# Kernel tuning notes

Hardware: AMD Instinct MI355X
Metric: run time of the kernel (lower is better)

Reference implementation:

```python
import jax, jax.numpy as jnp
import numpy as np

B, N, DH = 256, 32, 128      # batch, n_agents, per-agent hidden
E = 496                       # n_edges (fully connected over 32 agents)
DIM_IN = 2 * DH               # 256, MLP input (concat of two agent states)
DIM_HID = 256
A = 12                        # dim_act
R = 4                         # payoff_rank
DIM_OUT = 2 * R * A           # 96


def setup_inputs() -> dict:
    key = jax.random.key(0)
    ks = jax.random.split(key, 7)
    hidden_states_n = jax.random.normal(ks[0], (B, N, DH), dtype=jnp.float32)
    edges_from = jax.random.randint(ks[1], (E,), 0, N, dtype=jnp.int32).astype(jnp.int64)
    edges_to = jax.random.randint(ks[2], (E,), 0, N, dtype=jnp.int32).astype(jnp.int64)
    # torch.nn.Linear params: W [out, in], b [out]
    W1 = jax.random.normal(ks[3], (DIM_HID, DIM_IN), dtype=jnp.float32) * (1.0 / np.sqrt(DIM_IN))
    b1 = jnp.zeros((DIM_HID,), dtype=jnp.float32)
    W2 = jax.random.normal(ks[4], (DIM_OUT, DIM_HID), dtype=jnp.float32) * (1.0 / np.sqrt(DIM_HID))
    b2 = jnp.zeros((DIM_OUT,), dtype=jnp.float32)
    return {"hidden_states_n": hidden_states_n, "W1": W1, "b1": b1, "W2": W2,
            "b2": b2, "edges_from": edges_from, "edges_to": edges_to}


def reference(hidden_states_n, W1, b1, W2, b2, edges_from, edges_to):
    hf = hidden_states_n[:, edges_from]                     # [B, E, DH]
    ht = hidden_states_n[:, edges_to]                       # [B, E, DH]
    # stack of (from||to, to||from): [2, B, E, 2*DH]
    inp = jnp.stack([jnp.concatenate([hf, ht], axis=-1),
                     jnp.concatenate([ht, hf], axis=-1)], axis=0)
    h = jax.nn.relu(inp @ W1.T + b1)                        # [2, B, E, DIM_HID]
    p = h @ W2.T + b2                                       # [2, B, E, 2*R*A]
    p = p.reshape(2, B, E, R, 2, A)
    # low-rank outer product per rank, summed over ranks: [2, B, E, A, A]
    payoffs = jnp.einsum('sberi,sberj->sbeij', p[..., 0, :], p[..., 1, :])
    # second copy is transposed, then mean over the two directions
    return 0.5 * (payoffs[0] + jnp.swapaxes(payoffs[1], -1, -2))  # [B, E, A, A]
```

## Files before the change

kernel.cpp:

```cpp
#include <hip/hip_runtime.h>

typedef unsigned int uint;
typedef _Float16 f16;

typedef __attribute__((ext_vector_type(8))) _Float16 f16x8;
typedef __attribute__((ext_vector_type(2))) _Float16 f16x2;
typedef __attribute__((ext_vector_type(4))) float f32x4;

#define E_CNT 496

__device__ __forceinline__ uint pack2_f16(float lo, float hi) {
    union { f16x2 h; uint u; } r;
    r.h[0] = (_Float16)lo;
    r.h[1] = (_Float16)hi;
    return r.u;
}

__global__ __launch_bounds__(256) void x_kernel(
    const float* __restrict__ hidden, const float* __restrict__ W1,
    const float* __restrict__ b1, f16* __restrict__ Xout) {
    __shared__ __align__(16) float hs[64 * 132];

    const int tid = threadIdx.x;
    const int rowblock = blockIdx.x >> 2;
    const int g = blockIdx.x & 3;
    const int ln = tid & 63;
    const int waveId = tid >> 6;
    const int quad = ln >> 4;
    const int l16 = ln & 15;
    const int row0 = rowblock * 64;

    union FU { uint u[4]; f16x8 v; };
    FU wf[2][4];
    float bh[2][4];
    #pragma unroll
    for (int nt = 0; nt < 2; ++nt) {
        const int t = (g * 4 + waveId) * 2 + nt;
        const int half = t >> 4;
        const int htile = t & 15;
        const float* wrow = W1 + (htile * 16 + l16) * 256 + half * 128 + quad * 8;
        #pragma unroll
        for (int kk = 0; kk < 4; ++kk) {
            float4 v0 = *(const float4*)(wrow + kk * 32);
            float4 v1 = *(const float4*)(wrow + kk * 32 + 4);
            wf[nt][kk].u[0] = pack2_f16(v0.x, v0.y);
            wf[nt][kk].u[1] = pack2_f16(v0.z, v0.w);
            wf[nt][kk].u[2] = pack2_f16(v1.x, v1.y);
            wf[nt][kk].u[3] = pack2_f16(v1.z, v1.w);
        }
        #pragma unroll
        for (int r = 0; r < 4; ++r)
            bh[nt][r] = 0.5f * b1[htile * 16 + quad * 4 + r];
    }

    {
        const float* src = hidden + row0 * 128;
        #pragma unroll
        for (int it = 0; it < 8; ++it) {
            int idx = it * 256 + tid;
            int r = idx >> 5;
            int c4 = idx & 31;
            float4 v = *(const float4*)(src + idx * 4);
            *(float4*)&hs[r * 132 + c4 * 4] = v;
        }
    }
    __syncthreads();

    #pragma unroll
    for (int ch = 0; ch < 4; ++ch) {
        FU hf[4];
        const float* hrow = &hs[(ch * 16 + l16) * 132 + quad * 8];
        #pragma unroll
        for (int kk = 0; kk < 4; ++kk) {
            float4 v0 = *(const float4*)(hrow + kk * 32);
            float4 v1 = *(const float4*)(hrow + kk * 32 + 4);
            hf[kk].u[0] = pack2_f16(v0.x, v0.y);
            hf[kk].u[1] = pack2_f16(v0.z, v0.w);
            hf[kk].u[2] = pack2_f16(v1.x, v1.y);
            hf[kk].u[3] = pack2_f16(v1.z, v1.w);
        }
        #pragma unroll
        for (int nt = 0; nt < 2; ++nt) {
            const int t = (g * 4 + waveId) * 2 + nt;
            const int half = t >> 4;
            const int htile = t & 15;
            f32x4 acc = (f32x4){0.f, 0.f, 0.f, 0.f};
            #pragma unroll
            for (int kk = 0; kk < 4; ++kk)
                acc = __builtin_amdgcn_mfma_f32_16x16x32_f16(wf[nt][kk].v, hf[kk].v, acc, 0, 0, 0);
            uint2 o;
            o.x = pack2_f16(acc[0] + bh[nt][0], acc[1] + bh[nt][1]);
            o.y = pack2_f16(acc[2] + bh[nt][2], acc[3] + bh[nt][3]);
            f16* dst = Xout + half * (8192 * 256)
                     + (row0 + ch * 16 + l16) * 256 + htile * 16 + quad * 4;
            *(uint2*)dst = o;
        }
    }
}

#define PAIR_STRIDE 100
#define R_OFF 800
#define WAVE_PF 1600

__global__ __launch_bounds__(256, 4) void gemm_payoff_kernel(
    const f16* __restrict__ X1, const f16* __restrict__ X2,
    const int* __restrict__ e_f, const int* __restrict__ e_t,
    const float* __restrict__ W2, const float* __restrict__ b2,
    float* __restrict__ out) {

    __shared__ __align__(16) unsigned char smem[26624];
    f16* w2s = (f16*)smem;
    float* pf = (float*)smem;

    const int tid = threadIdx.x;
    const int ln = tid & 63;
    const int waveId = tid >> 6;
    const int quad = ln >> 4;
    const int l16 = ln & 15;
    const int pl = l16 & 7;
    const int s = l16 >> 3;

    const int bx = blockIdx.x;
    const int lb = (bx & 7) * 248 + (bx >> 3);

    bool f64 = true, t64 = true;
    #pragma unroll
    for (int i = 0; i < 16; ++i) {
        if (e_f[2 * i + 1] != 0) f64 = false;
        if (e_t[2 * i + 1] != 0) t64 = false;
    }

    const int pairBase = lb * 64 + waveId * 16;
    const f16* px1[2];
    const f16* px2[2];
    #pragma unroll
    for (int mt = 0; mt < 2; ++mt) {
        int pair = pairBase + mt * 8 + pl;
        int b = pair / E_CNT;
        int e = pair - b * E_CNT;
        int f = f64 ? e_f[2 * e] : e_f[e];
        int t = t64 ? e_t[2 * e] : e_t[e];
        int n1 = s ? t : f;
        int n2 = s ? f : t;
        px1[mt] = X1 + ((b * 32 + n1) * 256 + quad * 8);
        px2[mt] = X2 + ((b * 32 + n2) * 256 + quad * 8);
    }

    f32x4 acc[2][6];
    #pragma unroll
    for (int mt = 0; mt < 2; ++mt)
        #pragma unroll
        for (int tt = 0; tt < 6; ++tt) acc[mt][tt] = (f32x4){0.f, 0.f, 0.f, 0.f};

    typedef union { uint4 q; f16x8 h; } XU;
    XU G1[2][2], G2[2][2];

    #pragma unroll
    for (int mt = 0; mt < 2; ++mt) {
        G1[0][mt].q = *(const uint4*)(px1[mt] + 0 * 32);
        G2[0][mt].q = *(const uint4*)(px2[mt] + 0 * 32);
        G1[1][mt].q = *(const uint4*)(px1[mt] + 1 * 32);
        G2[1][mt].q = *(const uint4*)(px2[mt] + 1 * 32);
    }

    auto stageW2 = [&](int h) {
        #pragma unroll
        for (int j = 0; j < 12; ++j) {
            int idx4 = tid + j * 256;
            int n = idx4 >> 5;
            int k4 = idx4 & 31;
            float4 v = *(const float4*)&W2[n * 256 + h * 128 + k4 * 4];
            uint2 o;
            o.x = pack2_f16(v.x, v.y);
            o.y = pack2_f16(v.z, v.w);
            *(uint2*)&w2s[n * 136 + k4 * 4] = o;
        }
    };

    const f16x8 zero8 = (f16x8){0, 0, 0, 0, 0, 0, 0, 0};

    stageW2(0);
    __syncthreads();

    #pragma unroll
    for (int kk = 0; kk < 4; ++kk) {
        const int buf = kk & 1;
        f16x8 af[2];
        #pragma unroll
        for (int mt = 0; mt < 2; ++mt) {
            f16x8 sum = G1[buf][mt].h + G2[buf][mt].h;
            af[mt] = __builtin_elementwise_max(sum, zero8);
        }
        #pragma unroll
        for (int mt = 0; mt < 2; ++mt) {
            G1[buf][mt].q = *(const uint4*)(px1[mt] + (kk + 2) * 32);
            G2[buf][mt].q = *(const uint4*)(px2[mt] + (kk + 2) * 32);
        }
        #pragma unroll
        for (int tt = 0; tt < 6; ++tt) {
            f16x8 bf = *(const f16x8*)&w2s[(tt * 16 + l16) * 136 + kk * 32 + quad * 8];
            acc[0][tt] = __builtin_amdgcn_mfma_f32_16x16x32_f16(af[0], bf, acc[0][tt], 0, 0, 0);
            acc[1][tt] = __builtin_amdgcn_mfma_f32_16x16x32_f16(af[1], bf, acc[1][tt], 0, 0, 0);
        }
    }

    __syncthreads();
    stageW2(1);
    __syncthreads();

    #pragma unroll
    for (int kk = 4; kk < 8; ++kk) {
        const int buf = kk & 1;
        f16x8 af[2];
        #pragma unroll
        for (int mt = 0; mt < 2; ++mt) {
            f16x8 sum = G1[buf][mt].h + G2[buf][mt].h;
            af[mt] = __builtin_elementwise_max(sum, zero8);
        }
        if (kk < 6) {
            #pragma unroll
            for (int mt = 0; mt < 2; ++mt) {
                G1[buf][mt].q = *(const uint4*)(px1[mt] + (kk + 2) * 32);
                G2[buf][mt].q = *(const uint4*)(px2[mt] + (kk + 2) * 32);
            }
        }
        #pragma unroll
        for (int tt = 0; tt < 6; ++tt) {
            f16x8 bf = *(const f16x8*)&w2s[(tt * 16 + l16) * 136 + (kk - 4) * 32 + quad * 8];
            acc[0][tt] = __builtin_amdgcn_mfma_f32_16x16x32_f16(af[0], bf, acc[0][tt], 0, 0, 0);
            acc[1][tt] = __builtin_amdgcn_mfma_f32_16x16x32_f16(af[1], bf, acc[1][tt], 0, 0, 0);
        }
    }

    float b2v[6];
    #pragma unroll
    for (int tt = 0; tt < 6; ++tt) b2v[tt] = b2[tt * 16 + l16];

    int doff[6];
    {
        const int s_ = quad >> 1;
        #pragma unroll
        for (int tt = 0; tt < 6; ++tt) {
            int n = tt * 16 + l16;
            int rr = n / 24;
            int rem = n - rr * 24;
            int c01 = (rem >= 12) ? 1 : 0;
            int a = rem - c01 * 12;
            int k8 = (s_ ? 4 : 0) + rr;
            int toL = (c01 == s_) ? 1 : 0;
            doff[tt] = (toL ? 0 : R_OFF) + (quad & 1) * 4 * PAIR_STRIDE + a * 8 + k8;
        }
    }

    __syncthreads();

    float* wbase = pf + waveId * WAVE_PF;
    #pragma unroll
    for (int mt = 0; mt < 2; ++mt) {
        #pragma unroll
        for (int tt = 0; tt < 6; ++tt) {
            #pragma unroll
            for (int r = 0; r < 4; ++r) {
                wbase[doff[tt] + r * PAIR_STRIDE] = acc[mt][tt][r] + b2v[tt];
            }
        }

        #pragma unroll
        for (int it = 0; it < 2; ++it) {
            int task = it * 64 + ln;
            if (task < 96) {
                int pp = task / 12;
                int i = task - pp * 12;
                const float* Lp = wbase + pp * PAIR_STRIDE + i * 8;
                float4 l0 = *(const float4*)&Lp[0];
                float4 l1 = *(const float4*)&Lp[4];
                float od[12];
                #pragma unroll
                for (int jj = 0; jj < 12; ++jj) {
                    const float* Rp = wbase + R_OFF + pp * PAIR_STRIDE + jj * 8;
                    float4 r0 = *(const float4*)&Rp[0];
                    float4 r1 = *(const float4*)&Rp[4];
                    float d = l0.x * r0.x + l0.y * r0.y + l0.z * r0.z + l0.w * r0.w
                            + l1.x * r1.x + l1.y * r1.y + l1.z * r1.z + l1.w * r1.w;
                    od[jj] = 0.5f * d;
                }
                int outBase = (pairBase + mt * 8 + pp) * 144 + i * 12;
                *(float4*)&out[outBase + 0] = make_float4(od[0], od[1], od[2], od[3]);
                *(float4*)&out[outBase + 4] = make_float4(od[4], od[5], od[6], od[7]);
                *(float4*)&out[outBase + 8] = make_float4(od[8], od[9], od[10], od[11]);
            }
        }
    }
}

extern "C" void kernel_launch(void* const* d_in, const int* in_sizes, int n_in,
                              void* d_out, int out_size, void* d_ws, size_t ws_size,
                              hipStream_t stream) {
    const float* hidden = (const float*)d_in[0];
    const float* W1 = (const float*)d_in[1];
    const float* b1 = (const float*)d_in[2];
    const float* W2 = (const float*)d_in[3];
    const float* b2 = (const float*)d_in[4];
    const int* e_f = (const int*)d_in[5];
    const int* e_t = (const int*)d_in[6];
    float* out = (float*)d_out;

    char* ws = (char*)d_ws;
    f16* X = (f16*)ws;

    x_kernel<<<512, 256, 0, stream>>>(hidden, W1, b1, X);
    gemm_payoff_kernel<<<1984, 256, 0, stream>>>(X, X + 8192 * 256, e_f, e_t, W2, b2, out);
}
```

Before: 144.4 us.

## Pre-convert W2 to fp16 once, stage via direct LDS loads, MFMA payoff outer product

An extra block in the first kernel converts W2 to fp16 once into workspace, and the second kernel stages it into LDS with asynchronous global_load_lds instead of per-block fp32 load and convert. The first-half stage is issued at kernel start to overlap with index setup. The rank outer-product epilogue now stores p in fp16 and computes each 12x12 payoff with one MFMA per pair instead of scalar FMA dot products. This cuts redundant W2 conversion and epilogue ALU work, at the cost of fp16 rounding of p, a larger LDS footprint and wasted MFMA lanes.

Result: faster. 141.5 us (-2.0%).

```diff
diff --git a/kernel.cpp b/kernel.cpp
--- a/kernel.cpp
+++ b/kernel.cpp
@@ -8,6 +8,11 @@
 typedef __attribute__((ext_vector_type(4))) float f32x4;
 
 #define E_CNT 496
+
+#define W2_STRIDE 152
+#define W2_HALF_F16 (96 * W2_STRIDE)
+#define W2_HALF_BYTES (W2_HALF_F16 * 2)
+#define W2_CHUNKS 29
 
 __device__ __forceinline__ uint pack2_f16(float lo, float hi) {
     union { f16x2 h; uint u; } r;
@@ -16,12 +21,37 @@
     return r.u;
 }
 
+__device__ __forceinline__ void load_lds16(const void* g, void* l) {
+    __builtin_amdgcn_global_load_lds(
+        (const __attribute__((address_space(1))) void*)g,
+        (__attribute__((address_space(3))) void*)l, 16, 0, 0);
+}
+
 __global__ __launch_bounds__(256) void x_kernel(
     const float* __restrict__ hidden, const float* __restrict__ W1,
-    const float* __restrict__ b1, f16* __restrict__ Xout) {
+    const float* __restrict__ b1, f16* __restrict__ Xout,
+    const float* __restrict__ W2, f16* __restrict__ w2h) {
     __shared__ __align__(16) float hs[64 * 132];
 
     const int tid = threadIdx.x;
+
+    if (blockIdx.x == 512) {
+        #pragma unroll
+        for (int j = 0; j < 24; ++j) {
+            int idx4 = tid + j * 256;
+            int n = idx4 >> 6;
+            int k = (idx4 & 63) << 2;
+            int h = k >> 7;
+            int kin = k & 127;
+            float4 v = *(const float4*)&W2[n * 256 + k];
+            uint2 o;
+            o.x = pack2_f16(v.x, v.y);
+            o.y = pack2_f16(v.z, v.w);
+            *(uint2*)&w2h[h * W2_HALF_F16 + n * W2_STRIDE + kin] = o;
+        }
+        return;
+    }
+
     const int rowblock = blockIdx.x >> 2;
     const int g = blockIdx.x & 3;
     const int ln = tid & 63;
@@ -98,19 +128,14 @@
     }
 }
 
-#define PAIR_STRIDE 100
-#define R_OFF 800
-#define WAVE_PF 1600
-
 __global__ __launch_bounds__(256, 4) void gemm_payoff_kernel(
     const f16* __restrict__ X1, const f16* __restrict__ X2,
     const int* __restrict__ e_f, const int* __restrict__ e_t,
-    const float* __restrict__ W2, const float* __restrict__ b2,
+    const f16* __restrict__ w2g, const float* __restrict__ b2,
     float* __restrict__ out) {
 
-    __shared__ __align__(16) unsigned char smem[26624];
+    __shared__ __align__(16) unsigned char smem[32768];
     f16* w2s = (f16*)smem;
-    float* pf = (float*)smem;
 
     const int tid = threadIdx.x;
     const int ln = tid & 63;
@@ -122,6 +147,18 @@
 
     const int bx = blockIdx.x;
     const int lb = (bx & 7) * 248 + (bx >> 3);
+
+    auto stageW2 = [&](int h) {
+        const unsigned char* src = (const unsigned char*)w2g + h * W2_HALF_BYTES + ln * 16;
+        #pragma unroll
+        for (int j = 0; j < 8; ++j) {
+            int i = waveId + j * 4;
+            if (i < W2_CHUNKS)
+                load_lds16(src + i * 1024, smem + i * 1024);
+        }
+    };
+
+    stageW2(0);
 
     bool f64 = true, t64 = true;
     #pragma unroll
@@ -163,23 +200,8 @@
         G2[1][mt].q = *(const uint4*)(px2[mt] + 1 * 32);
     }
 
-    auto stageW2 = [&](int h) {
-        #pragma unroll
-        for (int j = 0; j < 12; ++j) {
-            int idx4 = tid + j * 256;
-            int n = idx4 >> 5;
-            int k4 = idx4 & 31;
-            float4 v = *(const float4*)&W2[n * 256 + h * 128 + k4 * 4];
-            uint2 o;
-            o.x = pack2_f16(v.x, v.y);
-            o.y = pack2_f16(v.z, v.w);
-            *(uint2*)&w2s[n * 136 + k4 * 4] = o;
-        }
-    };
-
     const f16x8 zero8 = (f16x8){0, 0, 0, 0, 0, 0, 0, 0};
 
-    stageW2(0);
     __syncthreads();
 
     #pragma unroll
@@ -198,7 +220,7 @@
         }
         #pragma unroll
         for (int tt = 0; tt < 6; ++tt) {
-            f16x8 bf = *(const f16x8*)&w2s[(tt * 16 + l16) * 136 + kk * 32 + quad * 8];
+            f16x8 bf = *(const f16x8*)&w2s[(tt * 16 + l16) * W2_STRIDE + kk * 32 + quad * 8];
             acc[0][tt] = __builtin_amdgcn_mfma_f32_16x16x32_f16(af[0], bf, acc[0][tt], 0, 0, 0);
             acc[1][tt] = __builtin_amdgcn_mfma_f32_16x16x32_f16(af[1], bf, acc[1][tt], 0, 0, 0);
         }
@@ -226,7 +248,7 @@
         }
         #pragma unroll
         for (int tt = 0; tt < 6; ++tt) {
-            f16x8 bf = *(const f16x8*)&w2s[(tt * 16 + l16) * 136 + (kk - 4) * 32 + quad * 8];
+            f16x8 bf = *(const f16x8*)&w2s[(tt * 16 + l16) * W2_STRIDE + (kk - 4) * 32 + quad * 8];
             acc[0][tt] = __builtin_amdgcn_mfma_f32_16x16x32_f16(af[0], bf, acc[0][tt], 0, 0, 0);
             acc[1][tt] = __builtin_amdgcn_mfma_f32_16x16x32_f16(af[1], bf, acc[1][tt], 0, 0, 0);
         }
@@ -236,7 +258,8 @@
     #pragma unroll
     for (int tt = 0; tt < 6; ++tt) b2v[tt] = b2[tt * 16 + l16];
 
-    int doff[6];
+    int d6[6];
+    float pscale[6];
     {
         const int s_ = quad >> 1;
         #pragma unroll
@@ -246,48 +269,38 @@
             int rem = n - rr * 24;
             int c01 = (rem >= 12) ? 1 : 0;
             int a = rem - c01 * 12;
-            int k8 = (s_ ? 4 : 0) + rr;
+            int k8 = s_ * 4 + rr;
             int toL = (c01 == s_) ? 1 : 0;
-            doff[tt] = (toL ? 0 : R_OFF) + (quad & 1) * 4 * PAIR_STRIDE + a * 8 + k8;
-        }
-    }
-
-    __syncthreads();
-
-    float* wbase = pf + waveId * WAVE_PF;
+            d6[tt] = (toL ? 0 : 1024) + (quad & 1) * 512 + a * 8 + k8;
+            pscale[tt] = toL ? 0.5f : 1.0f;
+        }
+    }
+
+    __syncthreads();
+
+    f16* pw = (f16*)smem + waveId * 4096;
     #pragma unroll
     for (int mt = 0; mt < 2; ++mt) {
+        f16* pm = pw + mt * 2048;
         #pragma unroll
         for (int tt = 0; tt < 6; ++tt) {
             #pragma unroll
-            for (int r = 0; r < 4; ++r) {
-                wbase[doff[tt] + r * PAIR_STRIDE] = acc[mt][tt][r] + b2v[tt];
+            for (int r = 0; r < 4; ++r)
+                pm[d6[tt] + r * 128] = (_Float16)((acc[mt][tt][r] + b2v[tt]) * pscale[tt]);
+        }
+        #pragma unroll
+        for (int pp = 0; pp < 8; ++pp) {
+            f16x8 afp = zero8, bfp = zero8;
+            if (quad == 0) {
+                afp = *(const f16x8*)&pm[pp * 128 + l16 * 8];
+                bfp = *(const f16x8*)&pm[1024 + pp * 128 + l16 * 8];
             }
-        }
-
-        #pragma unroll
-        for (int it = 0; it < 2; ++it) {
-            int task = it * 64 + ln;
-            if (task < 96) {
-                int pp = task / 12;
-                int i = task - pp * 12;
-                const float* Lp = wbase + pp * PAIR_STRIDE + i * 8;
-                float4 l0 = *(const float4*)&Lp[0];
-                float4 l1 = *(const float4*)&Lp[4];
-                float od[12];
+            f32x4 d = __builtin_amdgcn_mfma_f32_16x16x32_f16(
+                afp, bfp, (f32x4){0.f, 0.f, 0.f, 0.f}, 0, 0, 0);
+            if (l16 < 12 && quad < 3) {
+                float* ob = out + (pairBase + mt * 8 + pp) * 144 + quad * 48 + l16;
                 #pragma unroll
-                for (int jj = 0; jj < 12; ++jj) {
-                    const float* Rp = wbase + R_OFF + pp * PAIR_STRIDE + jj * 8;
-                    float4 r0 = *(const float4*)&Rp[0];
-                    float4 r1 = *(const float4*)&Rp[4];
-                    float d = l0.x * r0.x + l0.y * r0.y + l0.z * r0.z + l0.w * r0.w
-                            + l1.x * r1.x + l1.y * r1.y + l1.z * r1.z + l1.w * r1.w;
-                    od[jj] = 0.5f * d;
-                }
-                int outBase = (pairBase + mt * 8 + pp) * 144 + i * 12;
-                *(float4*)&out[outBase + 0] = make_float4(od[0], od[1], od[2], od[3]);
-                *(float4*)&out[outBase + 4] = make_float4(od[4], od[5], od[6], od[7]);
-                *(float4*)&out[outBase + 8] = make_float4(od[8], od[9], od[10], od[11]);
+                for (int r = 0; r < 4; ++r) ob[r * 12] = d[r];
             }
         }
     }
@@ -307,7 +320,8 @@
 
     char* ws = (char*)d_ws;
     f16* X = (f16*)ws;
-
-    x_kernel<<<512, 256, 0, stream>>>(hidden, W1, b1, X);
-    gemm_payoff_kernel<<<1984, 256, 0, stream>>>(X, X + 8192 * 256, e_f, e_t, W2, b2, out);
-}
+    f16* w2h = (f16*)(ws + 8 * 1024 * 1024);
+
+    x_kernel<<<513, 256, 0, stream>>>(hidden, W1, b1, X, W2, w2h);
+    gemm_payoff_kernel<<<1984, 256, 0, stream>>>(X, X + 8192 * 256, e_f, e_t, w2h, b2, out);
+}
```
